# Kernel tuning notes

Measured on AMD Instinct MI355X. Metric: run time of the kernel, lower is better.

Reference implementation:

```python
import jax, jax.numpy as jnp
import numpy as np

N_NODES = 50000
N_EDGES = 600000
IN_FEATS = 128
N_HIDDEN = 128
N_CLASSES = 40


def setup_inputs() -> dict:
    key = jax.random.key(0)
    ks = jax.random.split(key, 12)
    feat = jax.random.normal(ks[0], (N_NODES, IN_FEATS), dtype=jnp.float32)
    src = jax.random.randint(ks[1], (N_EDGES,), 0, N_NODES, dtype=jnp.int32)
    dst = jax.random.randint(ks[2], (N_EDGES,), 0, N_NODES, dtype=jnp.int32)
    dims = [(IN_FEATS, N_HIDDEN), (N_HIDDEN, N_HIDDEN), (N_HIDDEN, N_CLASSES)]
    params = {}
    for i, (di, do) in enumerate(dims):
        s = 1.0 / np.sqrt(di)
        params[f"w_self{i}"] = jax.random.uniform(ks[3 + 3 * i], (di, do), jnp.float32, -s, s)
        params[f"w_neigh{i}"] = jax.random.uniform(ks[4 + 3 * i], (di, do), jnp.float32, -s, s)
        params[f"b{i}"] = jnp.zeros((do,), jnp.float32)
    return dict(feat=feat, src=src, dst=dst, **params)


def _sage_layer(h, src, dst, w_self, w_neigh, b):
    # mean aggregation over in-neighbors: msg = h[src], reduce at dst
    msg_sum = jax.ops.segment_sum(h[src], dst, num_segments=N_NODES)  # [N, d]
    deg = jax.ops.segment_sum(jnp.ones((src.shape[0],), h.dtype), dst, num_segments=N_NODES)
    h_neigh = msg_sum / jnp.maximum(deg, 1.0)[:, None]
    # DGL SAGEConv(mean): out = fc_self(h) + fc_neigh(mean_neigh) + bias
    return h @ w_self + h_neigh @ w_neigh + b


def reference(feat, src, dst,
              w_self0, w_neigh0, b0,
              w_self1, w_neigh1, b1,
              w_self2, w_neigh2, b2):
    # dropout p=0.0 -> identity
    h = _sage_layer(feat, src, dst, w_self0, w_neigh0, b0)
    h = jax.nn.relu(h)
    h = _sage_layer(h, src, dst, w_self1, w_neigh1, b1)
    h = jax.nn.relu(h)
    h = _sage_layer(h, src, dst, w_self2, w_neigh2, b2)
    return h
```

## Files before the change

kernel.cpp:

```cpp
#include <hip/hip_runtime.h>

#define N_NODES 50000
#define N_EDGES 600000

typedef short bf16x8 __attribute__((ext_vector_type(8)));
typedef float f32x4  __attribute__((ext_vector_type(4)));
typedef unsigned short u16x8 __attribute__((ext_vector_type(8)));
typedef unsigned short u16x4 __attribute__((ext_vector_type(4)));

__device__ inline ushort rne_bf16(float a) {
    union { float f; unsigned u; } v; v.f = a;
    return (ushort)((v.u + 0x7FFFu + ((v.u >> 16) & 1u)) >> 16);
}
__device__ inline float bf16_to_f32(ushort h) {
    return __uint_as_float((unsigned)h << 16);
}
__device__ inline void split_bf16(float a, ushort& hi, ushort& lo) {
    hi = rne_bf16(a);
    float hv = bf16_to_f32(hi);
    lo = rne_bf16(a - hv);
}


__global__ void count_deg_kernel(const int* __restrict__ dst, int* __restrict__ deg, int ne) {
    int e = blockIdx.x * blockDim.x + threadIdx.x;
    if (e < ne) atomicAdd(&deg[dst[e]], 1);
}

__global__ __launch_bounds__(256) void block_sums_kernel(const int* __restrict__ deg,
                                                         int* __restrict__ bsum, int n) {
    __shared__ int s[256];
    int t = threadIdx.x;
    int i = blockIdx.x * 256 + t;
    s[t] = (i < n) ? deg[i] : 0;
    __syncthreads();
    #pragma unroll
    for (int d = 128; d > 0; d >>= 1) {
        if (t < d) s[t] += s[t + d];
        __syncthreads();
    }
    if (t == 0) bsum[blockIdx.x] = s[0];
}

__global__ __launch_bounds__(256) void scatter_fused_kernel(const int* __restrict__ deg,
                                                            const int* __restrict__ bsum,
                                                            int* __restrict__ off,
                                                            int* __restrict__ cur,
                                                            int n, int nb) {
    __shared__ int s[256];
    int t = threadIdx.x;

    int bv = (t < nb) ? bsum[t] : 0;
    s[t] = bv;
    __syncthreads();
    #pragma unroll
    for (int d = 1; d < 256; d <<= 1) {
        int x = (t >= d) ? s[t - d] : 0;
        __syncthreads();
        s[t] += x;
        __syncthreads();
    }
    int base = (blockIdx.x > 0) ? s[blockIdx.x - 1] : 0;
    if (blockIdx.x == 0 && t == 0) off[n] = s[255];
    __syncthreads();

    int i = blockIdx.x * 256 + t;
    int v = (i < n) ? deg[i] : 0;
    s[t] = v;
    __syncthreads();
    #pragma unroll
    for (int d = 1; d < 256; d <<= 1) {
        int x = (t >= d) ? s[t - d] : 0;
        __syncthreads();
        s[t] += x;
        __syncthreads();
    }
    if (i < n) {
        int excl = s[t] - v + base;
        off[i] = excl;
        cur[i] = excl;
    }
}

__global__ void fill_csr_kernel(const int* __restrict__ src, const int* __restrict__ dst,
                                int* __restrict__ cur, int* __restrict__ ssrc, int ne) {
    int e = blockIdx.x * blockDim.x + threadIdx.x;
    if (e < ne) {
        int p = atomicAdd(&cur[dst[e]], 1);
        ssrc[p] = src[e];
    }
}

__global__ void convert_all_w(const float* __restrict__ ws0, const float* __restrict__ wn0,
                              const float* __restrict__ ws1, const float* __restrict__ wn1,
                              const float* __restrict__ ws2, const float* __restrict__ wn2,
                              ushort* __restrict__ Bth0, ushort* __restrict__ Btl0,
                              ushort* __restrict__ Bth1, ushort* __restrict__ Btl1,
                              ushort* __restrict__ Bth2, ushort* __restrict__ Btl2) {
    int b = blockIdx.x;
    int k = threadIdx.x;
    const float *Ws, *Wn;
    ushort *H, *L;
    int dout, n;
    if (b < 256)      { n = b;       dout = 128; Ws = ws0; Wn = wn0; H = Bth0; L = Btl0; }
    else if (b < 512) { n = b - 256; dout = 128; Ws = ws1; Wn = wn1; H = Bth1; L = Btl1; }
    else              { n = b - 512; dout = 40;  Ws = ws2; Wn = wn2; H = Bth2; L = Btl2; }
    float w = (n < dout) ? Ws[(long)k * dout + n] : Wn[(long)k * dout + (n - dout)];
    ushort hi, lo;
    split_bf16(w, hi, lo);
    H[n * 128 + k] = hi;
    L[n * 128 + k] = lo;
}


#define KDIM 128
#define APAD 136

__device__ inline void stage_a_full(const float* __restrict__ A, int bm, int M, int tid,
                                    ushort* __restrict__ Ahi, ushort* __restrict__ Alo) {
    const int m  = tid >> 2;
    const int kq = (tid & 3) * 32;
    const int grow = bm + m;
    #pragma unroll
    for (int g = 0; g < 4; ++g) {
        float f[8];
        if (grow < M) {
            const float* ap = A + (long)grow * KDIM + kq + g * 8;
            float4 a0 = *(const float4*)ap;
            float4 a1 = *(const float4*)(ap + 4);
            f[0] = a0.x; f[1] = a0.y; f[2] = a0.z; f[3] = a0.w;
            f[4] = a1.x; f[5] = a1.y; f[6] = a1.z; f[7] = a1.w;
        } else {
            #pragma unroll
            for (int i = 0; i < 8; ++i) f[i] = 0.f;
        }
        ushort h[8], l[8];
        #pragma unroll
        for (int i = 0; i < 8; ++i) split_bf16(f[i], h[i], l[i]);
        uint4 hw, lw;
        hw.x = (unsigned)h[0] | ((unsigned)h[1] << 16);
        hw.y = (unsigned)h[2] | ((unsigned)h[3] << 16);
        hw.z = (unsigned)h[4] | ((unsigned)h[5] << 16);
        hw.w = (unsigned)h[6] | ((unsigned)h[7] << 16);
        lw.x = (unsigned)l[0] | ((unsigned)l[1] << 16);
        lw.y = (unsigned)l[2] | ((unsigned)l[3] << 16);
        lw.z = (unsigned)l[4] | ((unsigned)l[5] << 16);
        lw.w = (unsigned)l[6] | ((unsigned)l[7] << 16);
        *(uint4*)&Ahi[m * APAD + kq + g * 8] = hw;
        *(uint4*)&Alo[m * APAD + kq + g * 8] = lw;
    }
}

__global__ __launch_bounds__(256, 3) void gemm_mfma_wide(
    const float* __restrict__ A,
    const ushort* __restrict__ Bth, const ushort* __restrict__ Btl,
    const float* __restrict__ bias,
    float* __restrict__ S, ushort* __restrict__ T, int M)
{
    __shared__ ushort Ahi[64 * APAD];
    __shared__ ushort Alo[64 * APAD];

    const int tid = threadIdx.x;
    const int wave = tid >> 6;
    const int lane = tid & 63;
    const int lane16 = lane & 15;
    const int quad = lane >> 4;
    const int bm = blockIdx.x * 64;
    const int colbase = wave * 64;

    stage_a_full(A, bm, M, tid, Ahi, Alo);
    __syncthreads();

    const ushort* Bh0 = Bth + (long)(colbase + lane16) * KDIM + quad * 8;
    const ushort* Bl0 = Btl + (long)(colbase + lane16) * KDIM + quad * 8;

    f32x4 acc[4][4] = {};
    bf16x8 bhb[4], blb[4];

    #pragma unroll
    for (int p = 0; p < 3; ++p) {
        const int pc = p >> 2, pct = p & 3;
        bhb[p] = *(const bf16x8*)(Bh0 + pct * 16 * KDIM + pc * 32);
        blb[p] = *(const bf16x8*)(Bl0 + pct * 16 * KDIM + pc * 32);
    }

    bf16x8 ah[4], al[4];
    #pragma unroll
    for (int it = 0; it < 16; ++it) {
        const int c = it >> 2, ct = it & 3;
        if ((it & 3) == 0) {
            const int k0 = c * 32 + quad * 8;
            #pragma unroll
            for (int r = 0; r < 4; ++r) {
                int off = (16 * r + lane16) * APAD + k0;
                ah[r] = *(const bf16x8*)&Ahi[off];
                al[r] = *(const bf16x8*)&Alo[off];
            }
        }
        const int nx = it + 3;
        if (nx < 16) {
            const int nc = nx >> 2, nct = nx & 3;
            bhb[nx & 3] = *(const bf16x8*)(Bh0 + nct * 16 * KDIM + nc * 32);
            blb[nx & 3] = *(const bf16x8*)(Bl0 + nct * 16 * KDIM + nc * 32);
        }
        const bf16x8 bh = bhb[it & 3];
        const bf16x8 bl = blb[it & 3];
        #pragma unroll
        for (int r = 0; r < 4; ++r) {
            acc[r][ct] = __builtin_amdgcn_mfma_f32_16x16x32_bf16(bh, ah[r], acc[r][ct], 0, 0, 0);
            acc[r][ct] = __builtin_amdgcn_mfma_f32_16x16x32_bf16(bl, ah[r], acc[r][ct], 0, 0, 0);
            acc[r][ct] = __builtin_amdgcn_mfma_f32_16x16x32_bf16(bh, al[r], acc[r][ct], 0, 0, 0);
        }
    }

    #pragma unroll
    for (int ct = 0; ct < 4; ++ct) {
        const int col0 = colbase + 16 * ct + quad * 4;
        const bool toS = col0 < 128;
        f32x4 bv = {0,0,0,0};
        if (toS) bv = *(const f32x4*)(bias + col0);
        #pragma unroll
        for (int r = 0; r < 4; ++r) {
            const int row = bm + 16 * r + lane16;
            if (row < M) {
                if (toS) {
                    *(f32x4*)(S + (long)row * 128 + col0) = acc[r][ct] + bv;
                } else {
                    u16x4 t4;
                    #pragma unroll
                    for (int i = 0; i < 4; ++i) t4[i] = rne_bf16(acc[r][ct][i]);
                    *(u16x4*)(T + (long)row * 128 + (col0 - 128)) = t4;
                }
            }
        }
    }
}

__global__ __launch_bounds__(256, 3) void gemm_mfma_narrow(
    const float* __restrict__ A,
    const ushort* __restrict__ Bth, const ushort* __restrict__ Btl,
    const float* __restrict__ bias,
    float* __restrict__ S, ushort* __restrict__ T, int M)
{
    __shared__ ushort Ahi[64 * APAD];
    __shared__ ushort Alo[64 * APAD];

    const int tid = threadIdx.x;
    const int wave = tid >> 6;
    const int lane = tid & 63;
    const int lane16 = lane & 15;
    const int quad = lane >> 4;
    const int bm = blockIdx.x * 64;

    stage_a_full(A, bm, M, tid, Ahi, Alo);
    __syncthreads();

    const ushort* Bh0 = Bth + (long)lane16 * KDIM + quad * 8;
    const ushort* Bl0 = Btl + (long)lane16 * KDIM + quad * 8;

    f32x4 acc[5] = {};
    bf16x8 bhb[4], blb[4];

    #pragma unroll
    for (int p = 0; p < 3; ++p) {
        const int pc = p / 5, pct = p % 5;
        bhb[p] = *(const bf16x8*)(Bh0 + pct * 16 * KDIM + pc * 32);
        blb[p] = *(const bf16x8*)(Bl0 + pct * 16 * KDIM + pc * 32);
    }

    bf16x8 ah = {}, al = {};
    #pragma unroll
    for (int it = 0; it < 20; ++it) {
        const int c = it / 5, ct = it % 5;
        if (ct == 0) {
            const int off = (16 * wave + lane16) * APAD + c * 32 + quad * 8;
            ah = *(const bf16x8*)&Ahi[off];
            al = *(const bf16x8*)&Alo[off];
        }
        const int nx = it + 3;
        if (nx < 20) {
            const int nc = nx / 5, nct = nx % 5;
            bhb[nx & 3] = *(const bf16x8*)(Bh0 + nct * 16 * KDIM + nc * 32);
            blb[nx & 3] = *(const bf16x8*)(Bl0 + nct * 16 * KDIM + nc * 32);
        }
        const bf16x8 bh = bhb[it & 3];
        const bf16x8 bl = blb[it & 3];
        acc[ct] = __builtin_amdgcn_mfma_f32_16x16x32_bf16(bh, ah, acc[ct], 0, 0, 0);
        acc[ct] = __builtin_amdgcn_mfma_f32_16x16x32_bf16(bl, ah, acc[ct], 0, 0, 0);
        acc[ct] = __builtin_amdgcn_mfma_f32_16x16x32_bf16(bh, al, acc[ct], 0, 0, 0);
    }

    #pragma unroll
    for (int ct = 0; ct < 5; ++ct) {
        const int col0 = 16 * ct + quad * 4;
        const bool toS = col0 < 40;
        const int row = bm + 16 * wave + lane16;
        if (row < M) {
            if (toS) {
                f32x4 bv = *(const f32x4*)(bias + col0);
                *(f32x4*)(S + (long)row * 40 + col0) = acc[ct] + bv;
            } else {
                u16x4 t4;
                #pragma unroll
                for (int i = 0; i < 4; ++i) t4[i] = rne_bf16(acc[ct][i]);
                *(u16x4*)(T + (long)row * 40 + (col0 - 40)) = t4;
            }
        }
    }
}


template <int RELU>
__global__ __launch_bounds__(256) void agg128_kernel(
    const float* __restrict__ S, const ushort* __restrict__ T,
    const int* __restrict__ off, const int* __restrict__ ssrc,
    float* __restrict__ out, int nnodes)
{
    const int node = (blockIdx.x * 256 + threadIdx.x) >> 6;
    if (node >= nnodes) return;
    const int lane = threadIdx.x & 63;
    const int slot = lane >> 4;
    const int col8 = (lane & 15) * 8;

    const int a = off[node];
    const int b = off[node + 1];

    f32x4 acc0a = {0,0,0,0}, acc0b = {0,0,0,0};
    f32x4 acc1a = {0,0,0,0}, acc1b = {0,0,0,0};

    int i = a;
    for (; i + 8 <= b; i += 8) {
        int s0 = ssrc[i + slot];
        int s1 = ssrc[i + 4 + slot];
        u16x8 v0 = *(const u16x8*)(T + (long)s0 * 128 + col8);
        u16x8 v1 = *(const u16x8*)(T + (long)s1 * 128 + col8);
        #pragma unroll
        for (int j = 0; j < 4; ++j) {
            acc0a[j] += bf16_to_f32(v0[j]);
            acc0b[j] += bf16_to_f32(v0[4 + j]);
            acc1a[j] += bf16_to_f32(v1[j]);
            acc1b[j] += bf16_to_f32(v1[4 + j]);
        }
    }
    for (; i < b; i += 4) {
        int e = i + slot;
        if (e < b) {
            int s = ssrc[e];
            u16x8 v = *(const u16x8*)(T + (long)s * 128 + col8);
            #pragma unroll
            for (int j = 0; j < 4; ++j) {
                acc0a[j] += bf16_to_f32(v[j]);
                acc0b[j] += bf16_to_f32(v[4 + j]);
            }
        }
    }
    f32x4 accA = acc0a + acc1a;
    f32x4 accB = acc0b + acc1b;

    #pragma unroll
    for (int m = 16; m <= 32; m <<= 1) {
        #pragma unroll
        for (int j = 0; j < 4; ++j) {
            accA[j] += __shfl_xor((float)accA[j], m);
            accB[j] += __shfl_xor((float)accB[j], m);
        }
    }

    if (slot == 0) {
        int deg = b - a;
        float scale = (deg > 0) ? (1.0f / (float)deg) : 0.f;
        f32x4 sA = *(const f32x4*)(S + (long)node * 128 + col8);
        f32x4 sB = *(const f32x4*)(S + (long)node * 128 + col8 + 4);
        f32x4 rA = sA + accA * scale;
        f32x4 rB = sB + accB * scale;
        if (RELU) {
            #pragma unroll
            for (int j = 0; j < 4; ++j) {
                rA[j] = fmaxf(rA[j], 0.f);
                rB[j] = fmaxf(rB[j], 0.f);
            }
        }
        *(f32x4*)(out + (long)node * 128 + col8) = rA;
        *(f32x4*)(out + (long)node * 128 + col8 + 4) = rB;
    }
}

template <int RELU>
__global__ __launch_bounds__(256) void agg40_kernel(
    const float* __restrict__ S, const ushort* __restrict__ T,
    const int* __restrict__ off, const int* __restrict__ ssrc,
    float* __restrict__ out, int nnodes)
{
    const int node = (blockIdx.x * 256 + threadIdx.x) >> 6;
    if (node >= nnodes) return;
    const int lane = threadIdx.x & 63;
    const bool active = lane < 60;
    const int slot = active ? (lane / 10) : 5;
    const int fi = lane % 10;
    const int fo = fi * 4;

    const int a = off[node];
    const int b = off[node + 1];

    f32x4 acc0 = {0,0,0,0}, acc1 = {0,0,0,0};

    int i = a;
    for (; i + 12 <= b; i += 12) {
        int s0 = ssrc[i + slot];
        int s1 = ssrc[i + 6 + slot];
        u16x4 v0 = *(const u16x4*)(T + (long)s0 * 40 + fo);
        u16x4 v1 = *(const u16x4*)(T + (long)s1 * 40 + fo);
        if (active) {
            #pragma unroll
            for (int j = 0; j < 4; ++j) {
                acc0[j] += bf16_to_f32(v0[j]);
                acc1[j] += bf16_to_f32(v1[j]);
            }
        }
    }
    for (; i < b; i += 6) {
        int e = i + slot;
        if (active && e < b) {
            int s = ssrc[e];
            u16x4 v = *(const u16x4*)(T + (long)s * 40 + fo);
            #pragma unroll
            for (int j = 0; j < 4; ++j) acc0[j] += bf16_to_f32(v[j]);
        }
    }
    f32x4 acc = acc0 + acc1;

    f32x4 tot = acc;
    #pragma unroll
    for (int d = 10; d <= 50; d += 10) {
        int srcl = fi + d;
        #pragma unroll
        for (int j = 0; j < 4; ++j) tot[j] += __shfl((float)acc[j], srcl);
    }

    if (lane < 10) {
        int deg = b - a;
        float scale = (deg > 0) ? (1.0f / (float)deg) : 0.f;
        f32x4 s4 = *(const f32x4*)(S + (long)node * 40 + fo);
        f32x4 r = s4 + tot * scale;
        if (RELU) {
            #pragma unroll
            for (int j = 0; j < 4; ++j) r[j] = fmaxf(r[j], 0.f);
        }
        *(f32x4*)(out + (long)node * 40 + fo) = r;
    }
}


extern "C" void kernel_launch(void* const* d_in, const int* in_sizes, int n_in,
                              void* d_out, int out_size, void* d_ws, size_t ws_size,
                              hipStream_t stream) {
    const float* feat = (const float*)d_in[0];
    const int*   src  = (const int*)d_in[1];
    const int*   dst  = (const int*)d_in[2];
    const float* ws0  = (const float*)d_in[3];
    const float* wn0  = (const float*)d_in[4];
    const float* b0   = (const float*)d_in[5];
    const float* ws1  = (const float*)d_in[6];
    const float* wn1  = (const float*)d_in[7];
    const float* b1   = (const float*)d_in[8];
    const float* ws2  = (const float*)d_in[9];
    const float* wn2  = (const float*)d_in[10];
    const float* b2   = (const float*)d_in[11];

    const int N = N_NODES;
    const int NE = N_EDGES;
    const int NB = (N + 255) / 256;

    char* ws = (char*)d_ws;
    int*    offsets = (int*)(ws + 0);
    int*    cursor  = (int*)(ws + 200704);
    int*    degi    = (int*)(ws + 401408);
    int*    bsum    = (int*)(ws + 601600);
    int*    ssrc    = (int*)(ws + 603648);
    ushort* Bth0 = (ushort*)(ws + 200704);
    ushort* Btl0 = (ushort*)(ws + 266240);
    ushort* Bth1 = (ushort*)(ws + 331776);
    ushort* Btl1 = (ushort*)(ws + 397312);
    ushort* Bth2 = (ushort*)(ws + 462848);
    ushort* Btl2 = (ushort*)(ws + 483328);
    float*  hbuf = (float*)(ws + 3003904);
    float*  sbuf = (float*)(ws + 28603904);
    ushort* tbuf = (ushort*)(ws + 54203904);

    hipMemsetAsync(degi, 0, (size_t)N * sizeof(int), stream);
    count_deg_kernel<<<(NE + 255) / 256, 256, 0, stream>>>(dst, degi, NE);
    block_sums_kernel<<<NB, 256, 0, stream>>>(degi, bsum, N);
    scatter_fused_kernel<<<NB, 256, 0, stream>>>(degi, bsum, offsets, cursor, N, NB);
    fill_csr_kernel<<<(NE + 255) / 256, 256, 0, stream>>>(src, dst, cursor, ssrc, NE);

    convert_all_w<<<592, 128, 0, stream>>>(ws0, wn0, ws1, wn1, ws2, wn2,
                                           Bth0, Btl0, Bth1, Btl1, Bth2, Btl2);

    const int gx = (N + 63) / 64;
    const int ga = (N + 3) / 4;

    gemm_mfma_wide<<<gx, 256, 0, stream>>>(feat, Bth0, Btl0, b0, sbuf, tbuf, N);
    agg128_kernel<1><<<ga, 256, 0, stream>>>(sbuf, tbuf, offsets, ssrc, hbuf, N);

    gemm_mfma_wide<<<gx, 256, 0, stream>>>(hbuf, Bth1, Btl1, b1, sbuf, tbuf, N);
    agg128_kernel<1><<<ga, 256, 0, stream>>>(sbuf, tbuf, offsets, ssrc, hbuf, N);

    gemm_mfma_narrow<<<gx, 256, 0, stream>>>(hbuf, Bth2, Btl2, b2, sbuf, tbuf, N);
    agg40_kernel<0><<<ga, 256, 0, stream>>>(sbuf, tbuf, offsets, ssrc, (float*)d_out, N);
}
```

Measured before the change: 330.4 us.

## Halve GEMM row tile to 32 and redistribute narrow GEMM work across waves

Both MFMA GEMM kernels now stage 32-row A tiles instead of 64, doubling the grid and raising the occupancy hint from 3 to 4 blocks per CU. The wide kernel drops the software-pipelined B prefetch ring in favour of direct per-chunk B loads with fewer accumulators. The narrow kernel splits its 5 column tiles across wave pairs (3+2) over two 16-row groups instead of one wave per row group. This aims for more parallelism and lower register pressure, at the cost of more redundant B loads per output row and no explicit B prefetch.

New measurement: 335.2 us. No clear change (+1.5%).

```diff
diff --git a/kernel.cpp b/kernel.cpp
--- a/kernel.cpp
+++ b/kernel.cpp
@@ -116,100 +116,86 @@
 #define KDIM 128
 #define APAD 136
 
-__device__ inline void stage_a_full(const float* __restrict__ A, int bm, int M, int tid,
-                                    ushort* __restrict__ Ahi, ushort* __restrict__ Alo) {
-    const int m  = tid >> 2;
-    const int kq = (tid & 3) * 32;
+__device__ inline void stage_a32(const float* __restrict__ A, int bm, int M, int tid,
+                                 ushort* __restrict__ Ahi, ushort* __restrict__ Alo) {
+    const int m   = tid >> 3;
+    const int seg = (tid & 7) * 16;
     const int grow = bm + m;
-    #pragma unroll
-    for (int g = 0; g < 4; ++g) {
-        float f[8];
-        if (grow < M) {
-            const float* ap = A + (long)grow * KDIM + kq + g * 8;
-            float4 a0 = *(const float4*)ap;
-            float4 a1 = *(const float4*)(ap + 4);
-            f[0] = a0.x; f[1] = a0.y; f[2] = a0.z; f[3] = a0.w;
-            f[4] = a1.x; f[5] = a1.y; f[6] = a1.z; f[7] = a1.w;
-        } else {
-            #pragma unroll
-            for (int i = 0; i < 8; ++i) f[i] = 0.f;
-        }
-        ushort h[8], l[8];
-        #pragma unroll
-        for (int i = 0; i < 8; ++i) split_bf16(f[i], h[i], l[i]);
+    float f[16];
+    if (grow < M) {
+        const float* ap = A + (long)grow * KDIM + seg;
+        #pragma unroll
+        for (int q = 0; q < 4; ++q) {
+            float4 a = *(const float4*)(ap + q * 4);
+            f[q * 4 + 0] = a.x; f[q * 4 + 1] = a.y;
+            f[q * 4 + 2] = a.z; f[q * 4 + 3] = a.w;
+        }
+    } else {
+        #pragma unroll
+        for (int i = 0; i < 16; ++i) f[i] = 0.f;
+    }
+    ushort h[16], l[16];
+    #pragma unroll
+    for (int i = 0; i < 16; ++i) split_bf16(f[i], h[i], l[i]);
+    #pragma unroll
+    for (int q = 0; q < 2; ++q) {
         uint4 hw, lw;
-        hw.x = (unsigned)h[0] | ((unsigned)h[1] << 16);
-        hw.y = (unsigned)h[2] | ((unsigned)h[3] << 16);
-        hw.z = (unsigned)h[4] | ((unsigned)h[5] << 16);
-        hw.w = (unsigned)h[6] | ((unsigned)h[7] << 16);
-        lw.x = (unsigned)l[0] | ((unsigned)l[1] << 16);
-        lw.y = (unsigned)l[2] | ((unsigned)l[3] << 16);
-        lw.z = (unsigned)l[4] | ((unsigned)l[5] << 16);
-        lw.w = (unsigned)l[6] | ((unsigned)l[7] << 16);
-        *(uint4*)&Ahi[m * APAD + kq + g * 8] = hw;
-        *(uint4*)&Alo[m * APAD + kq + g * 8] = lw;
-    }
-}
-
-__global__ __launch_bounds__(256, 3) void gemm_mfma_wide(
+        hw.x = (unsigned)h[q*8+0] | ((unsigned)h[q*8+1] << 16);
+        hw.y = (unsigned)h[q*8+2] | ((unsigned)h[q*8+3] << 16);
+        hw.z = (unsigned)h[q*8+4] | ((unsigned)h[q*8+5] << 16);
+        hw.w = (unsigned)h[q*8+6] | ((unsigned)h[q*8+7] << 16);
+        lw.x = (unsigned)l[q*8+0] | ((unsigned)l[q*8+1] << 16);
+        lw.y = (unsigned)l[q*8+2] | ((unsigned)l[q*8+3] << 16);
+        lw.z = (unsigned)l[q*8+4] | ((unsigned)l[q*8+5] << 16);
+        lw.w = (unsigned)l[q*8+6] | ((unsigned)l[q*8+7] << 16);
+        *(uint4*)&Ahi[m * APAD + seg + q * 8] = hw;
+        *(uint4*)&Alo[m * APAD + seg + q * 8] = lw;
+    }
+}
+
+__global__ __launch_bounds__(256, 4) void gemm_mfma_wide(
     const float* __restrict__ A,
     const ushort* __restrict__ Bth, const ushort* __restrict__ Btl,
     const float* __restrict__ bias,
     float* __restrict__ S, ushort* __restrict__ T, int M)
 {
-    __shared__ ushort Ahi[64 * APAD];
-    __shared__ ushort Alo[64 * APAD];
+    __shared__ ushort Ahi[32 * APAD];
+    __shared__ ushort Alo[32 * APAD];
 
     const int tid = threadIdx.x;
     const int wave = tid >> 6;
     const int lane = tid & 63;
     const int lane16 = lane & 15;
     const int quad = lane >> 4;
-    const int bm = blockIdx.x * 64;
+    const int bm = blockIdx.x * 32;
     const int colbase = wave * 64;
 
-    stage_a_full(A, bm, M, tid, Ahi, Alo);
-    __syncthreads();
-
-    const ushort* Bh0 = Bth + (long)(colbase + lane16) * KDIM + quad * 8;
-    const ushort* Bl0 = Btl + (long)(colbase + lane16) * KDIM + quad * 8;
-
-    f32x4 acc[4][4] = {};
-    bf16x8 bhb[4], blb[4];
-
-    #pragma unroll
-    for (int p = 0; p < 3; ++p) {
-        const int pc = p >> 2, pct = p & 3;
-        bhb[p] = *(const bf16x8*)(Bh0 + pct * 16 * KDIM + pc * 32);
-        blb[p] = *(const bf16x8*)(Bl0 + pct * 16 * KDIM + pc * 32);
-    }
-
-    bf16x8 ah[4], al[4];
-    #pragma unroll
-    for (int it = 0; it < 16; ++it) {
-        const int c = it >> 2, ct = it & 3;
-        if ((it & 3) == 0) {
-            const int k0 = c * 32 + quad * 8;
-            #pragma unroll
-            for (int r = 0; r < 4; ++r) {
-                int off = (16 * r + lane16) * APAD + k0;
-                ah[r] = *(const bf16x8*)&Ahi[off];
-                al[r] = *(const bf16x8*)&Alo[off];
-            }
-        }
-        const int nx = it + 3;
-        if (nx < 16) {
-            const int nc = nx >> 2, nct = nx & 3;
-            bhb[nx & 3] = *(const bf16x8*)(Bh0 + nct * 16 * KDIM + nc * 32);
-            blb[nx & 3] = *(const bf16x8*)(Bl0 + nct * 16 * KDIM + nc * 32);
-        }
-        const bf16x8 bh = bhb[it & 3];
-        const bf16x8 bl = blb[it & 3];
-        #pragma unroll
-        for (int r = 0; r < 4; ++r) {
-            acc[r][ct] = __builtin_amdgcn_mfma_f32_16x16x32_bf16(bh, ah[r], acc[r][ct], 0, 0, 0);
-            acc[r][ct] = __builtin_amdgcn_mfma_f32_16x16x32_bf16(bl, ah[r], acc[r][ct], 0, 0, 0);
-            acc[r][ct] = __builtin_amdgcn_mfma_f32_16x16x32_bf16(bh, al[r], acc[r][ct], 0, 0, 0);
+    stage_a32(A, bm, M, tid, Ahi, Alo);
+    __syncthreads();
+
+    f32x4 acc[2][4] = {};
+
+    #pragma unroll
+    for (int c = 0; c < 4; ++c) {
+        const int k0 = c * 32 + quad * 8;
+        bf16x8 ah[2], al[2];
+        #pragma unroll
+        for (int r = 0; r < 2; ++r) {
+            int off = (16 * r + lane16) * APAD + k0;
+            ah[r] = *(const bf16x8*)&Ahi[off];
+            al[r] = *(const bf16x8*)&Alo[off];
+        }
+        #pragma unroll
+        for (int ct = 0; ct < 4; ++ct) {
+            const long boff = (long)(colbase + 16 * ct + lane16) * KDIM + k0;
+            bf16x8 bh = *(const bf16x8*)(Bth + boff);
+            bf16x8 bl = *(const bf16x8*)(Btl + boff);
+            #pragma unroll
+            for (int r = 0; r < 2; ++r) {
+                acc[r][ct] = __builtin_amdgcn_mfma_f32_16x16x32_bf16(bh, ah[r], acc[r][ct], 0, 0, 0);
+                acc[r][ct] = __builtin_amdgcn_mfma_f32_16x16x32_bf16(bl, ah[r], acc[r][ct], 0, 0, 0);
+                acc[r][ct] = __builtin_amdgcn_mfma_f32_16x16x32_bf16(bh, al[r], acc[r][ct], 0, 0, 0);
+            }
         }
     }
 
@@ -220,7 +206,7 @@
         f32x4 bv = {0,0,0,0};
         if (toS) bv = *(const f32x4*)(bias + col0);
         #pragma unroll
-        for (int r = 0; r < 4; ++r) {
+        for (int r = 0; r < 2; ++r) {
             const int row = bm + 16 * r + lane16;
             if (row < M) {
                 if (toS) {
@@ -236,74 +222,68 @@
     }
 }
 
-__global__ __launch_bounds__(256, 3) void gemm_mfma_narrow(
+__global__ __launch_bounds__(256, 4) void gemm_mfma_narrow(
     const float* __restrict__ A,
     const ushort* __restrict__ Bth, const ushort* __restrict__ Btl,
     const float* __restrict__ bias,
     float* __restrict__ S, ushort* __restrict__ T, int M)
 {
-    __shared__ ushort Ahi[64 * APAD];
-    __shared__ ushort Alo[64 * APAD];
+    __shared__ ushort Ahi[32 * APAD];
+    __shared__ ushort Alo[32 * APAD];
 
     const int tid = threadIdx.x;
     const int wave = tid >> 6;
     const int lane = tid & 63;
     const int lane16 = lane & 15;
     const int quad = lane >> 4;
-    const int bm = blockIdx.x * 64;
-
-    stage_a_full(A, bm, M, tid, Ahi, Alo);
-    __syncthreads();
-
-    const ushort* Bh0 = Bth + (long)lane16 * KDIM + quad * 8;
-    const ushort* Bl0 = Btl + (long)lane16 * KDIM + quad * 8;
-
-    f32x4 acc[5] = {};
-    bf16x8 bhb[4], blb[4];
-
-    #pragma unroll
-    for (int p = 0; p < 3; ++p) {
-        const int pc = p / 5, pct = p % 5;
-        bhb[p] = *(const bf16x8*)(Bh0 + pct * 16 * KDIM + pc * 32);
-        blb[p] = *(const bf16x8*)(Bl0 + pct * 16 * KDIM + pc * 32);
-    }
-
-    bf16x8 ah = {}, al = {};
-    #pragma unroll
-    for (int it = 0; it < 20; ++it) {
-        const int c = it / 5, ct = it % 5;
-        if (ct == 0) {
-            const int off = (16 * wave + lane16) * APAD + c * 32 + quad * 8;
-            ah = *(const bf16x8*)&Ahi[off];
-            al = *(const bf16x8*)&Alo[off];
-        }
-        const int nx = it + 3;
-        if (nx < 20) {
-            const int nc = nx / 5, nct = nx % 5;
-            bhb[nx & 3] = *(const bf16x8*)(Bh0 + nct * 16 * KDIM + nc * 32);
-            blb[nx & 3] = *(const bf16x8*)(Bl0 + nct * 16 * KDIM + nc * 32);
-        }
-        const bf16x8 bh = bhb[it & 3];
-        const bf16x8 bl = blb[it & 3];
-        acc[ct] = __builtin_amdgcn_mfma_f32_16x16x32_bf16(bh, ah, acc[ct], 0, 0, 0);
-        acc[ct] = __builtin_amdgcn_mfma_f32_16x16x32_bf16(bl, ah, acc[ct], 0, 0, 0);
-        acc[ct] = __builtin_amdgcn_mfma_f32_16x16x32_bf16(bh, al, acc[ct], 0, 0, 0);
-    }
-
-    #pragma unroll
-    for (int ct = 0; ct < 5; ++ct) {
-        const int col0 = 16 * ct + quad * 4;
-        const bool toS = col0 < 40;
-        const int row = bm + 16 * wave + lane16;
-        if (row < M) {
-            if (toS) {
-                f32x4 bv = *(const f32x4*)(bias + col0);
-                *(f32x4*)(S + (long)row * 40 + col0) = acc[ct] + bv;
-            } else {
-                u16x4 t4;
-                #pragma unroll
-                for (int i = 0; i < 4; ++i) t4[i] = rne_bf16(acc[ct][i]);
-                *(u16x4*)(T + (long)row * 40 + (col0 - 40)) = t4;
+    const int bm = blockIdx.x * 32;
+
+    const int rt = wave & 1;
+    const int cg = wave >> 1;
+    const int ctbase = cg * 3;
+    const int nct = cg ? 2 : 3;
+
+    stage_a32(A, bm, M, tid, Ahi, Alo);
+    __syncthreads();
+
+    f32x4 acc[3] = {};
+
+    #pragma unroll
+    for (int c = 0; c < 4; ++c) {
+        const int off = (rt * 16 + lane16) * APAD + c * 32 + quad * 8;
+        bf16x8 ah = *(const bf16x8*)&Ahi[off];
+        bf16x8 al = *(const bf16x8*)&Alo[off];
+        #pragma unroll
+        for (int j = 0; j < 3; ++j) {
+            if (j < nct) {
+                const int ct = ctbase + j;
+                const long boff = (long)(16 * ct + lane16) * KDIM + c * 32 + quad * 8;
+                bf16x8 bh = *(const bf16x8*)(Bth + boff);
+                bf16x8 bl = *(const bf16x8*)(Btl + boff);
+                acc[j] = __builtin_amdgcn_mfma_f32_16x16x32_bf16(bh, ah, acc[j], 0, 0, 0);
+                acc[j] = __builtin_amdgcn_mfma_f32_16x16x32_bf16(bl, ah, acc[j], 0, 0, 0);
+                acc[j] = __builtin_amdgcn_mfma_f32_16x16x32_bf16(bh, al, acc[j], 0, 0, 0);
+            }
+        }
+    }
+
+    #pragma unroll
+    for (int j = 0; j < 3; ++j) {
+        if (j < nct) {
+            const int ct = ctbase + j;
+            const int col0 = 16 * ct + quad * 4;
+            const bool toS = col0 < 40;
+            const int row = bm + rt * 16 + lane16;
+            if (row < M) {
+                if (toS) {
+                    f32x4 bv = *(const f32x4*)(bias + col0);
+                    *(f32x4*)(S + (long)row * 40 + col0) = acc[j] + bv;
+                } else {
+                    u16x4 t4;
+                    #pragma unroll
+                    for (int i = 0; i < 4; ++i) t4[i] = rne_bf16(acc[j][i]);
+                    *(u16x4*)(T + (long)row * 40 + (col0 - 40)) = t4;
+                }
             }
         }
     }
@@ -496,7 +476,7 @@
     convert_all_w<<<592, 128, 0, stream>>>(ws0, wn0, ws1, wn1, ws2, wn2,
                                            Bth0, Btl0, Bth1, Btl1, Bth2, Btl2);
 
-    const int gx = (N + 63) / 64;
+    const int gx = (N + 31) / 32;
     const int ga = (N + 3) / 4;
 
     gemm_mfma_wide<<<gx, 256, 0, stream>>>(feat, Bth0, Btl0, b0, sbuf, tbuf, N);
```
